# Kernel tuning notes

Measured on AMD Instinct MI355X. Metric: run time of the kernel, lower is better.

Reference implementation:

```python
import jax, jax.numpy as jnp
import numpy as np

N_NODES = 50000
LEAKY_SLOPE = 0.2


def _degrees(idx, n):
    d = jax.ops.segment_sum(jnp.ones_like(idx, dtype=jnp.float32), idx, num_segments=n)
    return jnp.clip(d, 1.0)  # DGL clamps zero degrees to 1


def _gcn_layer(x, W, b, src, dst, out_inv_sqrt, in_inv_sqrt):
    # norm='both': h = D_in^{-1/2} A D_out^{-1/2} x, then x @ W + b
    h = x * out_inv_sqrt[:, None]
    agg = jax.ops.segment_sum(jnp.take(h, src, axis=0), dst, num_segments=N_NODES)
    agg = agg * in_inv_sqrt[:, None]
    return agg @ W + b


def setup_inputs() -> dict:
    key = jax.random.key(0)
    k1, k2, k3, k4, k5 = jax.random.split(key, 5)
    E = 800000
    init_emb = jax.random.normal(k1, (N_NODES, 300), dtype=jnp.float32)
    W1 = jax.random.normal(k2, (300, 400), dtype=jnp.float32) * (1.0 / np.sqrt(300.0))
    b1 = jnp.zeros((400,), dtype=jnp.float32)
    W2 = jax.random.normal(k3, (400, 512), dtype=jnp.float32) * (1.0 / np.sqrt(400.0))
    b2 = jnp.zeros((512,), dtype=jnp.float32)
    src = jax.random.randint(k4, (E,), 0, N_NODES, dtype=jnp.int32)
    dst = jax.random.randint(k5, (E,), 0, N_NODES, dtype=jnp.int32)
    return {"init_emb": init_emb, "W1": W1, "b1": b1, "W2": W2, "b2": b2,
            "src": src, "dst": dst}


def reference(init_emb, W1, b1, W2, b2, src, dst):
    out_inv_sqrt = jax.lax.rsqrt(_degrees(src, N_NODES))  # D_out^{-1/2}
    in_inv_sqrt = jax.lax.rsqrt(_degrees(dst, N_NODES))   # D_in^{-1/2}
    x = _gcn_layer(init_emb, W1, b1, src, dst, out_inv_sqrt, in_inv_sqrt)
    x = jnp.where(x >= 0, x, LEAKY_SLOPE * x)  # LeakyReLU(0.2); dropout = identity (eval)
    x = _gcn_layer(x, W2, b2, src, dst, out_inv_sqrt, in_inv_sqrt)
    return x
```

## Files before the change

kernel.cpp:

```cpp
#include <hip/hip_runtime.h>
#include <hip/hip_fp16.h>

#define NN   50000
#define NNP  50048
#define D0   300
#define K1E  304
#define K1   320
#define N1   400
#define K2   448
#define N2   512
#define NBLK 196

typedef __attribute__((ext_vector_type(8))) short bf16x8;
typedef __attribute__((ext_vector_type(4))) float f32x4;
typedef __attribute__((ext_vector_type(2))) float f32x2;
typedef __attribute__((ext_vector_type(4))) unsigned int u32x4;

__device__ __forceinline__ unsigned short f2bf(float x) {
    union { float f; unsigned u; } v; v.f = x;
    unsigned r = v.u + 0x7fffu + ((v.u >> 16) & 1u);
    return (unsigned short)(r >> 16);
}

__global__ __launch_bounds__(256) void hist_kernel(const int* __restrict__ src,
                                                   const int* __restrict__ dst,
                                                   int* __restrict__ cnt_s,
                                                   int* __restrict__ cnt_d, int E) {
    int e = blockIdx.x * 256 + threadIdx.x;
    if (e < E) {
        atomicAdd(&cnt_s[src[e]], 1);
        atomicAdd(&cnt_d[dst[e]], 1);
    }
}

__global__ __launch_bounds__(256) void scan_blk_kernel(const int* __restrict__ cnt,
                                                       int* __restrict__ offs,
                                                       int* __restrict__ bsum) {
    __shared__ int sh[256];
    int t = threadIdx.x, g = blockIdx.x * 256 + t;
    int v = (g < NN) ? cnt[g] : 0;
    sh[t] = v;
    __syncthreads();
    for (int off = 1; off < 256; off <<= 1) {
        int u = (t >= off) ? sh[t - off] : 0;
        __syncthreads();
        sh[t] += u;
        __syncthreads();
    }
    if (g < NN) offs[g] = sh[t] - v;
    if (t == 255) bsum[blockIdx.x] = sh[255];
}

__global__ __launch_bounds__(256) void scan_top_kernel(const int* __restrict__ bsum,
                                                       int* __restrict__ boff) {
    __shared__ int sh[256];
    int t = threadIdx.x;
    int v = (t < NBLK) ? bsum[t] : 0;
    sh[t] = v;
    __syncthreads();
    for (int off = 1; off < 256; off <<= 1) {
        int u = (t >= off) ? sh[t - off] : 0;
        __syncthreads();
        sh[t] += u;
        __syncthreads();
    }
    if (t < NBLK) boff[t] = sh[t] - v;
}

__global__ __launch_bounds__(256) void scan_fix_kernel(int* __restrict__ offs,
                                                       const int* __restrict__ boff,
                                                       const int* __restrict__ cnt_s,
                                                       const int* __restrict__ cnt_d,
                                                       float* __restrict__ deg_s,
                                                       float* __restrict__ deg_d, int E) {
    int g = blockIdx.x * 256 + threadIdx.x;
    if (g < NN) {
        offs[g] += boff[blockIdx.x];
        deg_s[g] = rsqrtf(fmaxf((float)cnt_s[g], 1.0f));
        deg_d[g] = rsqrtf(fmaxf((float)cnt_d[g], 1.0f));
    }
    if (g == NN) offs[NN] = E;
}

__global__ __launch_bounds__(256) void scatter_kernel(const int* __restrict__ src,
                                                      const int* __restrict__ dst,
                                                      const int* __restrict__ offs,
                                                      int* __restrict__ cursor,
                                                      int* __restrict__ ssrc, int E) {
    int e = blockIdx.x * 256 + threadIdx.x;
    if (e < E) {
        int d = dst[e];
        int pos = atomicAdd(&cursor[d], 1);
        ssrc[offs[d] + pos] = src[e];
    }
}

__global__ __launch_bounds__(256) void embh_kernel(const float* __restrict__ emb,
                                                   const float* __restrict__ deg_s,
                                                   __half* __restrict__ embh) {
    int tid = blockIdx.x * 256 + threadIdx.x;
    const int CPR = K1E / 4;
    const int total = NN * CPR;
    if (tid >= total) return;
    int node = tid / CPR, c = tid - node * CPR;
    int f = 4 * c;
    __half h[4] = {__half(0.f), __half(0.f), __half(0.f), __half(0.f)};
    if (f < D0) {
        float sc = deg_s[node];
        float4 v = *(const float4*)(emb + (size_t)node * D0 + f);
        h[0] = __float2half(v.x * sc); h[1] = __float2half(v.y * sc);
        h[2] = __float2half(v.z * sc); h[3] = __float2half(v.w * sc);
    }
    *(uint2*)(embh + (size_t)node * K1E + f) = *(uint2*)h;
}

__global__ __launch_bounds__(256) void wt_kernel(const float* __restrict__ W1,
                                                 const float* __restrict__ W2,
                                                 unsigned short* __restrict__ T1,
                                                 unsigned short* __restrict__ T2) {
    int tid = blockIdx.x * 256 + threadIdx.x;
    if (tid < K2 * K1) {
        int n = tid / K1, k = tid - n * K1;
        float v = (n < N1 && k < D0) ? W1[k * N1 + n] : 0.f;
        T1[tid] = f2bf(v);
    } else {
        int u = tid - K2 * K1;
        if (u >= N2 * K2) return;
        int n = u / K2, k = u - n * K2;
        float v = (k < N1) ? W2[k * N2 + n] : 0.f;
        T2[u] = f2bf(v);
    }
}

template <int LD, int KP>
__global__ __launch_bounds__(256) void agg_h_kernel(
    const __half* __restrict__ X, const int* __restrict__ offs,
    const int* __restrict__ ssrc, const float* __restrict__ nscale,
    unsigned short* __restrict__ O) {
    constexpr int D8 = LD / 8;
    constexpr int O8 = KP / 8;
    int node = blockIdx.x * 4 + (threadIdx.x >> 6);
    if (node >= NNP) return;
    int l = threadIdx.x & 63;
    bool act = l < D8;
    const uint4* Xq = (const uint4*)X;

    float a[8] = {0.f, 0.f, 0.f, 0.f, 0.f, 0.f, 0.f, 0.f};

#define ACCUM(U) { const __half2* hp = (const __half2*)&(U);                        \
                   float2 f0 = __half22float2(hp[0]), f1 = __half22float2(hp[1]);   \
                   float2 f2 = __half22float2(hp[2]), f3 = __half22float2(hp[3]);   \
                   a[0] += f0.x; a[1] += f0.y; a[2] += f1.x; a[3] += f1.y;          \
                   a[4] += f2.x; a[5] += f2.y; a[6] += f3.x; a[7] += f3.y; }

    if (node < NN) {
        int j = offs[node], end = offs[node + 1];
        for (; j + 8 <= end; j += 8) {
            uint4 u0, u1, u2, u3, u4, u5, u6, u7;
            int s0 = ssrc[j + 0], s1 = ssrc[j + 1], s2 = ssrc[j + 2], s3 = ssrc[j + 3];
            int s4 = ssrc[j + 4], s5 = ssrc[j + 5], s6 = ssrc[j + 6], s7 = ssrc[j + 7];
            if (act) {
                u0 = Xq[(size_t)s0 * D8 + l]; u1 = Xq[(size_t)s1 * D8 + l];
                u2 = Xq[(size_t)s2 * D8 + l]; u3 = Xq[(size_t)s3 * D8 + l];
                u4 = Xq[(size_t)s4 * D8 + l]; u5 = Xq[(size_t)s5 * D8 + l];
                u6 = Xq[(size_t)s6 * D8 + l]; u7 = Xq[(size_t)s7 * D8 + l];
                ACCUM(u0); ACCUM(u1); ACCUM(u2); ACCUM(u3);
                ACCUM(u4); ACCUM(u5); ACCUM(u6); ACCUM(u7);
            }
        }
        for (; j + 2 <= end; j += 2) {
            int s0 = ssrc[j + 0], s1 = ssrc[j + 1];
            if (act) {
                uint4 u0 = Xq[(size_t)s0 * D8 + l];
                uint4 u1 = Xq[(size_t)s1 * D8 + l];
                ACCUM(u0); ACCUM(u1);
            }
        }
        for (; j < end; ++j) {
            int s0 = ssrc[j];
            if (act) { uint4 u0 = Xq[(size_t)s0 * D8 + l]; ACCUM(u0); }
        }
        float ns = nscale[node];
#pragma unroll
        for (int i = 0; i < 8; ++i) a[i] *= ns;
    }
#undef ACCUM

    if (l < O8) {
        unsigned short hv[8];
#pragma unroll
        for (int i = 0; i < 8; ++i) hv[i] = f2bf(a[i]);
        __builtin_nontemporal_store(*(u32x4*)hv, (u32x4*)(O + (size_t)node * KP + 8 * l));
    }
}

__global__ __launch_bounds__(256) void agg_q_kernel(
    const unsigned char* __restrict__ X, const int* __restrict__ offs,
    const int* __restrict__ ssrc, const float* __restrict__ nscale,
    unsigned short* __restrict__ O) {
    constexpr int D16 = 25;
    constexpr int OS  = 28;
    int w = threadIdx.x >> 6, l = threadIdx.x & 63;
    int half = l >> 5, sl = l & 31;
    int node = blockIdx.x * 8 + w * 2 + half;
    bool act = sl < D16;
    const uint4* Xq = (const uint4*)X;

    float a[16];
#pragma unroll
    for (int i = 0; i < 16; ++i) a[i] = 0.f;

#define ACCQ(U) { f32x2 p;                                                          \
    p = __builtin_amdgcn_cvt_pk_f32_fp8((int)(U).x, false); a[0]+=p.x;  a[1]+=p.y;  \
    p = __builtin_amdgcn_cvt_pk_f32_fp8((int)(U).x, true);  a[2]+=p.x;  a[3]+=p.y;  \
    p = __builtin_amdgcn_cvt_pk_f32_fp8((int)(U).y, false); a[4]+=p.x;  a[5]+=p.y;  \
    p = __builtin_amdgcn_cvt_pk_f32_fp8((int)(U).y, true);  a[6]+=p.x;  a[7]+=p.y;  \
    p = __builtin_amdgcn_cvt_pk_f32_fp8((int)(U).z, false); a[8]+=p.x;  a[9]+=p.y;  \
    p = __builtin_amdgcn_cvt_pk_f32_fp8((int)(U).z, true);  a[10]+=p.x; a[11]+=p.y; \
    p = __builtin_amdgcn_cvt_pk_f32_fp8((int)(U).w, false); a[12]+=p.x; a[13]+=p.y; \
    p = __builtin_amdgcn_cvt_pk_f32_fp8((int)(U).w, true);  a[14]+=p.x; a[15]+=p.y; }

    if (node < NN) {
        int j = offs[node], end = offs[node + 1];
        for (; j + 8 <= end; j += 8) {
            uint4 u0, u1, u2, u3, u4, u5, u6, u7;
            int s0 = ssrc[j + 0], s1 = ssrc[j + 1], s2 = ssrc[j + 2], s3 = ssrc[j + 3];
            int s4 = ssrc[j + 4], s5 = ssrc[j + 5], s6 = ssrc[j + 6], s7 = ssrc[j + 7];
            if (act) {
                u0 = Xq[(size_t)s0 * D16 + sl]; u1 = Xq[(size_t)s1 * D16 + sl];
                u2 = Xq[(size_t)s2 * D16 + sl]; u3 = Xq[(size_t)s3 * D16 + sl];
                u4 = Xq[(size_t)s4 * D16 + sl]; u5 = Xq[(size_t)s5 * D16 + sl];
                u6 = Xq[(size_t)s6 * D16 + sl]; u7 = Xq[(size_t)s7 * D16 + sl];
                ACCQ(u0); ACCQ(u1); ACCQ(u2); ACCQ(u3);
                ACCQ(u4); ACCQ(u5); ACCQ(u6); ACCQ(u7);
            }
        }
        for (; j + 2 <= end; j += 2) {
            int s0 = ssrc[j + 0], s1 = ssrc[j + 1];
            if (act) {
                uint4 u0 = Xq[(size_t)s0 * D16 + sl];
                uint4 u1 = Xq[(size_t)s1 * D16 + sl];
                ACCQ(u0); ACCQ(u1);
            }
        }
        for (; j < end; ++j) {
            int s0 = ssrc[j];
            if (act) { uint4 u0 = Xq[(size_t)s0 * D16 + sl]; ACCQ(u0); }
        }
        float ns = nscale[node];
#pragma unroll
        for (int i = 0; i < 16; ++i) a[i] *= ns;
    }
#undef ACCQ

    if (node < NNP && sl < OS) {
        unsigned short hv[16];
#pragma unroll
        for (int i = 0; i < 16; ++i) hv[i] = f2bf(a[i]);
        unsigned short* dst = O + (size_t)node * K2 + 16 * sl;
        __builtin_nontemporal_store(*(u32x4*)hv, (u32x4*)dst);
        __builtin_nontemporal_store(*(u32x4*)(hv + 8), (u32x4*)(dst + 8));
    }
}

template <int OMODE>
__global__ __launch_bounds__(256) void gemm_bf16_kernel(
    const unsigned short* __restrict__ A, const unsigned short* __restrict__ BT,
    const float* __restrict__ bias, const float* __restrict__ rs,
    void* __restrict__ Cv, int nbn, int Kpad, int Nvalid, int Cld) {
    __shared__ unsigned short lds[12288];
    const int AOF = 0, BOF = 8192;

    int nwg = (int)gridDim.x, orig = (int)blockIdx.x;
    int q8 = nwg >> 3, r8 = nwg & 7;
    int xc = orig & 7, o8 = orig >> 3;
    int wg = (xc < r8 ? xc * (q8 + 1) : r8 * (q8 + 1) + (xc - r8) * q8) + o8;
    int bn = wg % nbn, bm = wg / nbn;
    int m0 = bm * 128, n0 = bn * 64;

    int t = threadIdx.x, l = t & 63, w = t >> 6;
    int wm = w >> 1, wn = w & 1;

    f32x4 acc[4][2] = {};

    for (int k0 = 0; k0 < Kpad; k0 += 64) {
#pragma unroll
        for (int j = 0; j < 4; ++j) {
            int c = j * 256 + t;
            int r = c >> 3, qs = c & 7;
            size_t goff = (size_t)(m0 + r) * Kpad + k0 + ((qs ^ (r & 7)) << 3);
            int lbase = (j * 256 + w * 64) * 8;
            __builtin_amdgcn_global_load_lds(
                (const __attribute__((address_space(1))) void*)(A + goff),
                (__attribute__((address_space(3))) void*)&lds[AOF + lbase], 16, 0, 0);
        }
#pragma unroll
        for (int j = 0; j < 2; ++j) {
            int c = j * 256 + t;
            int r = c >> 3, qs = c & 7;
            size_t goff = (size_t)(n0 + r) * Kpad + k0 + ((qs ^ (r & 7)) << 3);
            int lbase = (j * 256 + w * 64) * 8;
            __builtin_amdgcn_global_load_lds(
                (const __attribute__((address_space(1))) void*)(BT + goff),
                (__attribute__((address_space(3))) void*)&lds[BOF + lbase], 16, 0, 0);
        }
        __syncthreads();

#pragma unroll
        for (int ks = 0; ks < 2; ++ks) {
            bf16x8 bfr[2];
#pragma unroll
            for (int ni = 0; ni < 2; ++ni) {
                int n = wn * 32 + ni * 16 + (l & 15);
                int slot = ks * 4 + (l >> 4);
                int idx = n * 64 + ((slot ^ (n & 7)) << 3);
                bfr[ni] = *(const bf16x8*)&lds[BOF + idx];
            }
#pragma unroll
            for (int mi = 0; mi < 4; ++mi) {
                int m = wm * 64 + mi * 16 + (l & 15);
                int slot = ks * 4 + (l >> 4);
                int idx = m * 64 + ((slot ^ (m & 7)) << 3);
                bf16x8 afr = *(const bf16x8*)&lds[AOF + idx];
#pragma unroll
                for (int ni = 0; ni < 2; ++ni)
                    acc[mi][ni] = __builtin_amdgcn_mfma_f32_16x16x32_bf16(afr, bfr[ni], acc[mi][ni], 0, 0, 0);
            }
        }
        __syncthreads();
    }

#pragma unroll
    for (int mi = 0; mi < 4; ++mi) {
        int mbase = m0 + wm * 64 + mi * 16 + ((l >> 4) << 2);
#pragma unroll
        for (int q = 0; q < 4; ++q) {
            int m = mbase + q;
            if (m >= NN) continue;
            float scale = (OMODE == 1) ? rs[m] : 1.0f;
#pragma unroll
            for (int ni = 0; ni < 2; ++ni) {
                int n = n0 + wn * 32 + ni * 16 + (l & 15);
                if (n >= Nvalid) continue;
                float v = acc[mi][ni][q] + bias[n];
                if (OMODE == 1) {
                    v = v >= 0.f ? v : 0.2f * v;
                    v *= scale;
                    int pk = __builtin_amdgcn_cvt_pk_fp8_f32(v, v, 0, false);
                    ((unsigned char*)Cv)[(size_t)m * Cld + n] = (unsigned char)(pk & 0xff);
                } else {
                    ((float*)Cv)[(size_t)m * Cld + n] = v;
                }
            }
        }
    }
}

extern "C" void kernel_launch(void* const* d_in, const int* in_sizes, int n_in,
                              void* d_out, int out_size, void* d_ws, size_t ws_size,
                              hipStream_t stream) {
    const float* emb = (const float*)d_in[0];
    const float* W1  = (const float*)d_in[1];
    const float* b1  = (const float*)d_in[2];
    const float* W2  = (const float*)d_in[3];
    const float* b2  = (const float*)d_in[4];
    const int*   src = (const int*)d_in[5];
    const int*   dst = (const int*)d_in[6];
    const int E = in_sizes[5];

    unsigned short* A1   = (unsigned short*)d_ws;
    unsigned short* A2   = A1 + (size_t)NNP * K1;
    __half*         embh = (__half*)A2;
    unsigned short* W1T  = A2 + (size_t)NNP * K2;
    unsigned short* W2T  = W1T + (size_t)K2 * K1;

    unsigned char* h2  = (unsigned char*)d_out;
    float*         out = (float*)d_out;
    char* tail = (char*)d_out + (size_t)NN * N1;
    int* cnt_s  = (int*)tail;
    int* cnt_d  = cnt_s + NN;
    int* cursor = cnt_d + NN;
    int* offs   = cursor + NN;
    int* bsum   = offs + NN + 1;
    int* boff   = bsum + NBLK;
    int* ssrc   = boff + NBLK;
    float* deg_s = (float*)(ssrc + E);
    float* deg_d = deg_s + NN;

    hipMemsetAsync(cnt_s, 0, (size_t)(3 * NN) * sizeof(int), stream);

    hist_kernel<<<(E + 255) / 256, 256, 0, stream>>>(src, dst, cnt_s, cnt_d, E);
    scan_blk_kernel<<<NBLK, 256, 0, stream>>>(cnt_d, offs, bsum);
    scan_top_kernel<<<1, 256, 0, stream>>>(bsum, boff);
    scan_fix_kernel<<<NBLK, 256, 0, stream>>>(offs, boff, cnt_s, cnt_d, deg_s, deg_d, E);
    scatter_kernel<<<(E + 255) / 256, 256, 0, stream>>>(src, dst, offs, cursor, ssrc, E);

    embh_kernel<<<(NN * (K1E / 4) + 255) / 256, 256, 0, stream>>>(emb, deg_s, embh);
    wt_kernel<<<(K2 * K1 + N2 * K2 + 255) / 256, 256, 0, stream>>>(W1, W2, W1T, W2T);

    agg_h_kernel<K1E, K1><<<NNP / 4, 256, 0, stream>>>(embh, offs, ssrc, deg_d, A1);

    gemm_bf16_kernel<1><<<391 * 7, 256, 0, stream>>>(
        A1, W1T, b1, deg_s, h2, 7, K1, N1, N1);

    agg_q_kernel<<<NNP / 8, 256, 0, stream>>>(h2, offs, ssrc, deg_d, A2);

    gemm_bf16_kernel<0><<<391 * 8, 256, 0, stream>>>(
        A2, W2T, b2, nullptr, out, 8, K2, N2, N2);
}
```

Before: 392.9 us.

## Double-buffer GEMM LDS tiles and fuse histogram with weight transpose

The bf16 GEMM now uses two LDS buffers and issues the next K-tile's global-to-LDS loads before computing the current tile, so memory latency can overlap with MFMA work. The histogram and weight-transpose kernels are merged into one launch to save a kernel launch. The final fp32 output stores become nontemporal. Doubling LDS to 48KB per block may reduce the number of resident workgroups.

Result: slower. 422.4 us (+7.5%).

```diff
diff --git a/kernel.cpp b/kernel.cpp
--- a/kernel.cpp
+++ b/kernel.cpp
@@ -22,14 +22,31 @@
     return (unsigned short)(r >> 16);
 }
 
-__global__ __launch_bounds__(256) void hist_kernel(const int* __restrict__ src,
-                                                   const int* __restrict__ dst,
-                                                   int* __restrict__ cnt_s,
-                                                   int* __restrict__ cnt_d, int E) {
-    int e = blockIdx.x * 256 + threadIdx.x;
-    if (e < E) {
-        atomicAdd(&cnt_s[src[e]], 1);
-        atomicAdd(&cnt_d[dst[e]], 1);
+__global__ __launch_bounds__(256) void pre_kernel(const int* __restrict__ src,
+                                                  const int* __restrict__ dst,
+                                                  int* __restrict__ cnt_s,
+                                                  int* __restrict__ cnt_d, int E,
+                                                  const float* __restrict__ W1,
+                                                  const float* __restrict__ W2,
+                                                  unsigned short* __restrict__ T1,
+                                                  unsigned short* __restrict__ T2) {
+    int tid = blockIdx.x * 256 + threadIdx.x;
+    if (tid < E) {
+        atomicAdd(&cnt_s[src[tid]], 1);
+        atomicAdd(&cnt_d[dst[tid]], 1);
+        return;
+    }
+    int u = tid - E;
+    if (u < K2 * K1) {
+        int n = u / K1, k = u - n * K1;
+        float v = (n < N1 && k < D0) ? W1[k * N1 + n] : 0.f;
+        T1[u] = f2bf(v);
+    } else {
+        u -= K2 * K1;
+        if (u >= N2 * K2) return;
+        int n = u / K2, k = u - n * K2;
+        float v = (k < N1) ? W2[k * N2 + n] : 0.f;
+        T2[u] = f2bf(v);
     }
 }
 
@@ -114,24 +131,6 @@
     *(uint2*)(embh + (size_t)node * K1E + f) = *(uint2*)h;
 }
 
-__global__ __launch_bounds__(256) void wt_kernel(const float* __restrict__ W1,
-                                                 const float* __restrict__ W2,
-                                                 unsigned short* __restrict__ T1,
-                                                 unsigned short* __restrict__ T2) {
-    int tid = blockIdx.x * 256 + threadIdx.x;
-    if (tid < K2 * K1) {
-        int n = tid / K1, k = tid - n * K1;
-        float v = (n < N1 && k < D0) ? W1[k * N1 + n] : 0.f;
-        T1[tid] = f2bf(v);
-    } else {
-        int u = tid - K2 * K1;
-        if (u >= N2 * K2) return;
-        int n = u / K2, k = u - n * K2;
-        float v = (k < N1) ? W2[k * N2 + n] : 0.f;
-        T2[u] = f2bf(v);
-    }
-}
-
 template <int LD, int KP>
 __global__ __launch_bounds__(256) void agg_h_kernel(
     const __half* __restrict__ X, const int* __restrict__ offs,
@@ -268,8 +267,7 @@
     const unsigned short* __restrict__ A, const unsigned short* __restrict__ BT,
     const float* __restrict__ bias, const float* __restrict__ rs,
     void* __restrict__ Cv, int nbn, int Kpad, int Nvalid, int Cld) {
-    __shared__ unsigned short lds[12288];
-    const int AOF = 0, BOF = 8192;
+    __shared__ unsigned short lds[24576];
 
     int nwg = (int)gridDim.x, orig = (int)blockIdx.x;
     int q8 = nwg >> 3, r8 = nwg & 7;
@@ -283,45 +281,53 @@
 
     f32x4 acc[4][2] = {};
 
-    for (int k0 = 0; k0 < Kpad; k0 += 64) {
+    auto stage = [&](int b, int k0) {
 #pragma unroll
         for (int j = 0; j < 4; ++j) {
             int c = j * 256 + t;
             int r = c >> 3, qs = c & 7;
             size_t goff = (size_t)(m0 + r) * Kpad + k0 + ((qs ^ (r & 7)) << 3);
-            int lbase = (j * 256 + w * 64) * 8;
+            int lbase = b * 12288 + (j * 256 + w * 64) * 8;
             __builtin_amdgcn_global_load_lds(
                 (const __attribute__((address_space(1))) void*)(A + goff),
-                (__attribute__((address_space(3))) void*)&lds[AOF + lbase], 16, 0, 0);
+                (__attribute__((address_space(3))) void*)&lds[lbase], 16, 0, 0);
         }
 #pragma unroll
         for (int j = 0; j < 2; ++j) {
             int c = j * 256 + t;
             int r = c >> 3, qs = c & 7;
             size_t goff = (size_t)(n0 + r) * Kpad + k0 + ((qs ^ (r & 7)) << 3);
-            int lbase = (j * 256 + w * 64) * 8;
+            int lbase = b * 12288 + 8192 + (j * 256 + w * 64) * 8;
             __builtin_amdgcn_global_load_lds(
                 (const __attribute__((address_space(1))) void*)(BT + goff),
-                (__attribute__((address_space(3))) void*)&lds[BOF + lbase], 16, 0, 0);
-        }
-        __syncthreads();
-
+                (__attribute__((address_space(3))) void*)&lds[lbase], 16, 0, 0);
+        }
+    };
+
+    const int NK = Kpad >> 6;
+    stage(0, 0);
+    __syncthreads();
+
+    for (int ki = 0; ki < NK; ++ki) {
+        int cur = ki & 1;
+        if (ki + 1 < NK) stage(cur ^ 1, (ki + 1) << 6);
+
+        int ab = cur * 12288, bb = cur * 12288 + 8192;
 #pragma unroll
         for (int ks = 0; ks < 2; ++ks) {
+            int slot = ks * 4 + (l >> 4);
             bf16x8 bfr[2];
 #pragma unroll
             for (int ni = 0; ni < 2; ++ni) {
                 int n = wn * 32 + ni * 16 + (l & 15);
-                int slot = ks * 4 + (l >> 4);
                 int idx = n * 64 + ((slot ^ (n & 7)) << 3);
-                bfr[ni] = *(const bf16x8*)&lds[BOF + idx];
+                bfr[ni] = *(const bf16x8*)&lds[bb + idx];
             }
 #pragma unroll
             for (int mi = 0; mi < 4; ++mi) {
                 int m = wm * 64 + mi * 16 + (l & 15);
-                int slot = ks * 4 + (l >> 4);
                 int idx = m * 64 + ((slot ^ (m & 7)) << 3);
-                bf16x8 afr = *(const bf16x8*)&lds[AOF + idx];
+                bf16x8 afr = *(const bf16x8*)&lds[ab + idx];
 #pragma unroll
                 for (int ni = 0; ni < 2; ++ni)
                     acc[mi][ni] = __builtin_amdgcn_mfma_f32_16x16x32_bf16(afr, bfr[ni], acc[mi][ni], 0, 0, 0);
@@ -349,7 +355,7 @@
                     int pk = __builtin_amdgcn_cvt_pk_fp8_f32(v, v, 0, false);
                     ((unsigned char*)Cv)[(size_t)m * Cld + n] = (unsigned char)(pk & 0xff);
                 } else {
-                    ((float*)Cv)[(size_t)m * Cld + n] = v;
+                    __builtin_nontemporal_store(v, (float*)Cv + (size_t)m * Cld + n);
                 }
             }
         }
@@ -389,14 +395,17 @@
 
     hipMemsetAsync(cnt_s, 0, (size_t)(3 * NN) * sizeof(int), stream);
 
-    hist_kernel<<<(E + 255) / 256, 256, 0, stream>>>(src, dst, cnt_s, cnt_d, E);
+    {
+        int total = E + K2 * K1 + N2 * K2;
+        pre_kernel<<<(total + 255) / 256, 256, 0, stream>>>(
+            src, dst, cnt_s, cnt_d, E, W1, W2, W1T, W2T);
+    }
     scan_blk_kernel<<<NBLK, 256, 0, stream>>>(cnt_d, offs, bsum);
     scan_top_kernel<<<1, 256, 0, stream>>>(bsum, boff);
     scan_fix_kernel<<<NBLK, 256, 0, stream>>>(offs, boff, cnt_s, cnt_d, deg_s, deg_d, E);
     scatter_kernel<<<(E + 255) / 256, 256, 0, stream>>>(src, dst, offs, cursor, ssrc, E);
 
     embh_kernel<<<(NN * (K1E / 4) + 255) / 256, 256, 0, stream>>>(emb, deg_s, embh);
-    wt_kernel<<<(K2 * K1 + N2 * K2 + 255) / 256, 256, 0, stream>>>(W1, W2, W1T, W2T);
 
     agg_h_kernel<K1E, K1><<<NNP / 4, 256, 0, stream>>>(embh, offs, ssrc, deg_d, A1);
 
```
